# Optimization experiments

Measured on AMD Instinct MI355X. Metric: run time of the kernel, lower is better.

Reference implementation:

```python
import jax, jax.numpy as jnp
import numpy as np

DT = 1.0
TOL = 2e-4
MAX_FK = 0.1


def _lap(x):
    # 5-point Laplacian with periodic boundary (roll-based), x: [B,1,H,W]
    return (jnp.roll(x, 1, -1) + jnp.roll(x, -1, -1)
            + jnp.roll(x, 1, -2) + jnp.roll(x, -1, -2) - 4.0 * x)


def _gs_step(u, v, Du, Dv, F, k, dt):
    uvv = u * v * v
    u_next = u + dt * (Du * _lap(u) - uvv + F * (1.0 - u))
    v_next = v + dt * (Dv * _lap(v) + uvv - (F + k) * v)
    return u_next, v_next


def setup_inputs() -> dict:
    key = jax.random.key(0)
    k1, k2 = jax.random.split(key)
    B, H, W = 32, 512, 512
    # physically sensible Gray-Scott init: u near 1, v small
    u = 1.0 - 0.5 * jax.random.uniform(k1, (B, 1, H, W), dtype=jnp.float32)
    v = 0.25 * jax.random.uniform(k2, (B, 1, H, W), dtype=jnp.float32)
    return {
        "u": u,
        "v": v,
        "log_Du": jnp.float32(-2.0),
        "log_Dv": jnp.float32(-2.0),
        "raw_F": jnp.float32(0.0),
        "raw_k": jnp.float32(0.0),
        "max_steps": 64,
        "K": 32,
    }


def reference(u, v, log_Du, log_Dv, raw_F, raw_k, max_steps, K):
    # params_tensor()
    Du = jax.nn.softplus(log_Du)
    Dv = jax.nn.softplus(log_Dv)
    F = MAX_FK * jax.nn.sigmoid(raw_F)
    k = MAX_FK * jax.nn.sigmoid(raw_k)

    B = u.shape[0]
    converged0 = jnp.zeros((B,), dtype=bool)

    # Phase 1: simulate-until-converged (per-sample freeze), expressed as a
    # fixed-length masked scan (no data-dependent shapes). Samples that were
    # already converged at the start of a step keep their state frozen,
    # matching the index_select/scatter semantics of the torch loop.
    def steady_body(carry, _):
        u, v, conv = carry
        u_next, v_next = _gs_step(u, v, Du, Dv, F, k, DT)
        du = jnp.max(jnp.abs(u_next - u), axis=(1, 2, 3))
        dv = jnp.max(jnp.abs(v_next - v), axis=(1, 2, 3))
        newly = jnp.maximum(du, dv) < TOL
        m = conv[:, None, None, None]
        u2 = jnp.where(m, u, u_next)
        v2 = jnp.where(m, v, v_next)
        return (u2, v2, conv | newly), None

    (u, v, converged), _ = jax.lax.scan(
        steady_body, (u, v, converged0), None, length=max_steps)

    # Phase 2: K differentiable steps (trunc BPTT segment), no masking
    def bptt_body(carry, _):
        u, v = carry
        return _gs_step(u, v, Du, Dv, F, k, DT), None

    (u, v), _ = jax.lax.scan(bptt_body, (u, v), None, length=K)
    return (u, v)
```

## Files before the change

### kernel.cpp

```cpp
#include <hip/hip_runtime.h>

#define HH 512
#define WW 512
#define BB 32
#define NIMG (HH * WW)
#define NT (BB * NIMG)
#define TOLF 0.0002f
#define HS 32
#define NSTRIP (HH / HS)
#define TRP 16
#define TIP (TRP + 2)
#define NTBP (HH / TRP)

__device__ __forceinline__ void gs_math(
    const float4& cu, const float4& uu, const float4& ud, float ul, float ur,
    const float4& cv, const float4& vu, const float4& vd, float vl, float vr,
    float Du, float Dv, float F, float Fk, float4& un, float4& vn)
{
    float4 lu, lv;
    lu.x = ul   + cu.y + uu.x + ud.x - 4.f * cu.x;
    lu.y = cu.x + cu.z + uu.y + ud.y - 4.f * cu.y;
    lu.z = cu.y + cu.w + uu.z + ud.z - 4.f * cu.z;
    lu.w = cu.z + ur   + uu.w + ud.w - 4.f * cu.w;
    lv.x = vl   + cv.y + vu.x + vd.x - 4.f * cv.x;
    lv.y = cv.x + cv.z + vu.y + vd.y - 4.f * cv.y;
    lv.z = cv.y + cv.w + vu.z + vd.z - 4.f * cv.z;
    lv.w = cv.z + vr   + vu.w + vd.w - 4.f * cv.w;
    float uvv;
    uvv  = cu.x * cv.x * cv.x;
    un.x = cu.x + (Du * lu.x - uvv + F * (1.f - cu.x));
    vn.x = cv.x + (Dv * lv.x + uvv - Fk * cv.x);
    uvv  = cu.y * cv.y * cv.y;
    un.y = cu.y + (Du * lu.y - uvv + F * (1.f - cu.y));
    vn.y = cv.y + (Dv * lv.y + uvv - Fk * cv.y);
    uvv  = cu.z * cv.z * cv.z;
    un.z = cu.z + (Du * lu.z - uvv + F * (1.f - cu.z));
    vn.z = cv.z + (Dv * lv.z + uvv - Fk * cv.z);
    uvv  = cu.w * cv.w * cv.w;
    un.w = cu.w + (Du * lu.w - uvv + F * (1.f - cu.w));
    vn.w = cv.w + (Dv * lv.w + uvv - Fk * cv.w);
}

__device__ __forceinline__ float dmax8(const float4& un, const float4& cu,
                                       const float4& vn, const float4& cv)
{
    return fmaxf(
        fmaxf(fmaxf(fabsf(un.x - cu.x), fabsf(un.y - cu.y)),
              fmaxf(fabsf(un.z - cu.z), fabsf(un.w - cu.w))),
        fmaxf(fmaxf(fabsf(vn.x - cv.x), fabsf(vn.y - cv.y)),
              fmaxf(fabsf(vn.z - cv.z), fabsf(vn.w - cv.w))));
}

__device__ __forceinline__ int s5(int r) { int m = r % 5; return m < 0 ? m + 5 : m; }

__device__ __forceinline__ void produce_ring(
    const float (* __restrict__ Su)[WW], const float (* __restrict__ Sv)[WW],
    float (* __restrict__ Tu)[WW], float (* __restrict__ Tv)[WW],
    int r, int c0, float Du, float Dv, float F, float Fk, float& dm, bool acc)
{
    const int sm = s5(r - 1), s0 = s5(r), sp = s5(r + 1);
    const int cl = (c0 - 4) & (WW - 1), cr = (c0 + 4) & (WW - 1);
    const float4 cu = *(const float4*)&Su[s0][c0];
    const float4 uu = *(const float4*)&Su[sm][c0];
    const float4 ud = *(const float4*)&Su[sp][c0];
    const float  ul = ((const float4*)&Su[s0][cl])->w;
    const float  ur = ((const float4*)&Su[s0][cr])->x;
    const float4 cv = *(const float4*)&Sv[s0][c0];
    const float4 vu = *(const float4*)&Sv[sm][c0];
    const float4 vd = *(const float4*)&Sv[sp][c0];
    const float  vl = ((const float4*)&Sv[s0][cl])->w;
    const float  vr = ((const float4*)&Sv[s0][cr])->x;
    float4 un, vn;
    gs_math(cu, uu, ud, ul, ur, cv, vu, vd, vl, vr, Du, Dv, F, Fk, un, vn);
    *(float4*)&Tu[s0][c0] = un;
    *(float4*)&Tv[s0][c0] = vn;
    if (acc) dm = fmaxf(dm, dmax8(un, cu, vn, cv));
}

__global__ __launch_bounds__(256)
void gs_quad(const float* __restrict__ fsU, const float* __restrict__ fsV,
             float* wsU, float* wsV, float* outU, float* outV,
             const float* __restrict__ consts,
             const int* __restrict__ conv, const int* __restrict__ par,
             float* __restrict__ pmax, int tpar, int steady)
{
    __shared__ float Iu[5][WW], Iv[5][WW], Au[5][WW], Av[5][WW],
                     Bu[5][WW], Bv[5][WW], Cu[5][WW], Cv[5][WW];

    const int b = blockIdx.y;
    if (steady && conv[b]) return;
    const int p = par[b] ^ tpar;
    const float* __restrict__ su = p ? outU : wsU;
    const float* __restrict__ sv = p ? outV : wsV;
    float* __restrict__ dU = p ? wsU : outU;
    float* __restrict__ dV = p ? wsV : outV;
    if (fsU) { su = fsU; sv = fsV; }

    const float Du = consts[0], Dv = consts[1], F = consts[2], Fk = consts[3];
    const int t  = threadIdx.x;
    const int rw = t >> 7;
    const int c0 = (t & 127) * 4;
    const int R0 = blockIdx.x * HS;
    const size_t ib = (size_t)b * NIMG;

    float d1 = 0.f, d2 = 0.f, d3 = 0.f, d4 = 0.f;

    float4 pu, pv;
    {   const int g = (R0 - 4 + rw) & (HH - 1);
        pu = *(const float4*)(su + ib + (size_t)g * WW + c0);
        pv = *(const float4*)(sv + ib + (size_t)g * WW + c0);
    }

    for (int i = 0; i < 24; ++i) {
        const int rI = 2*i - 4  + rw;
        const int rA = 2*i - 6  + rw;
        const int rB = 2*i - 10 + rw;
        const int rC = 2*i - 12 + rw;
        const int rO = 2*i - 16 + rw;

        if (rI <= HS + 3) {
            const int s = s5(rI);
            *(float4*)&Iu[s][c0] = pu;
            *(float4*)&Iv[s][c0] = pv;
        }
        if (rB >= -2 && rB <= HS + 1)
            produce_ring(Au, Av, Bu, Bv, rB, c0, Du, Dv, F, Fk, d2,
                         steady && rB >= 0 && rB < HS);
        if (rO >= 0 && rO < HS) {
            const int sm = s5(rO - 1), s0 = s5(rO), sp = s5(rO + 1);
            const int cl = (c0 - 4) & (WW - 1), cr = (c0 + 4) & (WW - 1);
            const float4 cu = *(const float4*)&Cu[s0][c0];
            const float4 uu = *(const float4*)&Cu[sm][c0];
            const float4 ud = *(const float4*)&Cu[sp][c0];
            const float  ul = ((const float4*)&Cu[s0][cl])->w;
            const float  ur = ((const float4*)&Cu[s0][cr])->x;
            const float4 cv = *(const float4*)&Cv[s0][c0];
            const float4 vu = *(const float4*)&Cv[sm][c0];
            const float4 vd = *(const float4*)&Cv[sp][c0];
            const float  vl = ((const float4*)&Cv[s0][cl])->w;
            const float  vr = ((const float4*)&Cv[s0][cr])->x;
            float4 un, vn;
            gs_math(cu, uu, ud, ul, ur, cv, vu, vd, vl, vr, Du, Dv, F, Fk, un, vn);
            *(float4*)(dU + ib + (size_t)(R0 + rO) * WW + c0) = un;
            *(float4*)(dV + ib + (size_t)(R0 + rO) * WW + c0) = vn;
            if (steady) d4 = fmaxf(d4, dmax8(un, cu, vn, cv));
        }
        __syncthreads();

        {   const int rn = 2*i - 2 + rw;
            if (rn <= HS + 3) {
                const int g = (R0 + rn) & (HH - 1);
                pu = *(const float4*)(su + ib + (size_t)g * WW + c0);
                pv = *(const float4*)(sv + ib + (size_t)g * WW + c0);
            }
        }

        if (rA >= -3 && rA <= HS + 2)
            produce_ring(Iu, Iv, Au, Av, rA, c0, Du, Dv, F, Fk, d1,
                         steady && rA >= 0 && rA < HS);
        if (rC >= -1 && rC <= HS)
            produce_ring(Bu, Bv, Cu, Cv, rC, c0, Du, Dv, F, Fk, d3,
                         steady && rC >= 0 && rC < HS);
        __syncthreads();
    }

    if (steady) {
        #pragma unroll
        for (int off = 1; off < 64; off <<= 1) {
            d1 = fmaxf(d1, __shfl_xor(d1, off));
            d2 = fmaxf(d2, __shfl_xor(d2, off));
            d3 = fmaxf(d3, __shfl_xor(d3, off));
            d4 = fmaxf(d4, __shfl_xor(d4, off));
        }
        const int w = t >> 6;
        if ((t & 63) == 0) {
            Iu[0][w * 4 + 0] = d1; Iu[0][w * 4 + 1] = d2;
            Iu[0][w * 4 + 2] = d3; Iu[0][w * 4 + 3] = d4;
        }
        __syncthreads();
        if (t == 0) {
            float m0 = 0.f, m1 = 0.f, m2 = 0.f, m3 = 0.f;
            #pragma unroll
            for (int w2 = 0; w2 < 4; ++w2) {
                m0 = fmaxf(m0, Iu[0][w2 * 4 + 0]);
                m1 = fmaxf(m1, Iu[0][w2 * 4 + 1]);
                m2 = fmaxf(m2, Iu[0][w2 * 4 + 2]);
                m3 = fmaxf(m3, Iu[0][w2 * 4 + 3]);
            }
            const int idx = b * NSTRIP + blockIdx.x;
            pmax[0 * BB * NSTRIP + idx] = m0;
            pmax[1 * BB * NSTRIP + idx] = m1;
            pmax[2 * BB * NSTRIP + idx] = m2;
            pmax[3 * BB * NSTRIP + idx] = m3;
        }
    }
}

__global__ void gs_upd(const int* __restrict__ convO, const int* __restrict__ parO,
                       int* convN, int* parN, int* rbJ,
                       const float* __restrict__ pmax)
{
    const int b = blockIdx.x, t = threadIdx.x;
    if (convO[b]) { if (t == 0) { convN[b] = 1; parN[b] = parO[b]; rbJ[b] = 0; } return; }
    float v0 = 0.f, v1 = 0.f, v2 = 0.f, v3 = 0.f;
    if (t < NSTRIP) {
        const int idx = b * NSTRIP + t;
        v0 = pmax[0 * BB * NSTRIP + idx];
        v1 = pmax[1 * BB * NSTRIP + idx];
        v2 = pmax[2 * BB * NSTRIP + idx];
        v3 = pmax[3 * BB * NSTRIP + idx];
    }
    #pragma unroll
    for (int off = 1; off < NSTRIP; off <<= 1) {
        v0 = fmaxf(v0, __shfl_xor(v0, off));
        v1 = fmaxf(v1, __shfl_xor(v1, off));
        v2 = fmaxf(v2, __shfl_xor(v2, off));
        v3 = fmaxf(v3, __shfl_xor(v3, off));
    }
    if (t == 0) {
        int j = 0;
        if      (v0 < TOLF) j = 1;
        else if (v1 < TOLF) j = 2;
        else if (v2 < TOLF) j = 3;
        else if (v3 < TOLF) j = 4;
        const int pO = parO[b];
        convN[b] = (j != 0);
        parN[b]  = (j == 3) ? pO : (pO ^ 1);
        rbJ[b]   = (j >= 1 && j <= 3) ? j : 0;
    }
}

__device__ __forceinline__ void load_row(const float* __restrict__ s,
                                         int base, int baseUp, int baseDn, int c0,
                                         float4& c, float4& up, float4& dn, float& l, float& r)
{
    c  = *(const float4*)(s + base   + c0);
    up = *(const float4*)(s + baseUp + c0);
    dn = *(const float4*)(s + baseDn + c0);
    l  = s[base + ((c0 - 1) & (WW - 1))];
    r  = s[base + ((c0 + 4) & (WW - 1))];
}

__global__ __launch_bounds__(256)
void gs_rollA(const float* __restrict__ fsU, const float* __restrict__ fsV,
              float* wsU, float* wsV, float* outU, float* outV,
              const float* __restrict__ consts,
              const int* __restrict__ parO, const int* __restrict__ rbJ)
{
    __shared__ float iu[TIP][WW];
    __shared__ float iv[TIP][WW];
    const int b = blockIdx.y;
    if (rbJ[b] < 2) return;
    const int p = parO[b];
    const float* __restrict__ su = p ? outU : wsU;
    const float* __restrict__ sv = p ? outV : wsV;
    float* __restrict__ dU = p ? wsU : outU;
    float* __restrict__ dV = p ? wsV : outV;
    if (fsU) { su = fsU; sv = fsV; }
    const float Du = consts[0], Dv = consts[1], F = consts[2], Fk = consts[3];
    const int t = threadIdx.x, c0 = (t & 127) * 4, rw = t >> 7;
    const int r0 = blockIdx.x * TRP;
    for (int i = 0; i < TIP; i += 2) {
        const int li = i + rw;
        const int h  = (r0 - 1 + li) & (HH - 1);
        const int hm = (h - 1) & (HH - 1);
        const int hp = (h + 1) & (HH - 1);
        const int base   = b * NIMG + h  * WW;
        const int baseUp = b * NIMG + hm * WW;
        const int baseDn = b * NIMG + hp * WW;
        float4 cu, uu, ud, cv, vu, vd; float ul, ur, vl, vr;
        load_row(su, base, baseUp, baseDn, c0, cu, uu, ud, ul, ur);
        load_row(sv, base, baseUp, baseDn, c0, cv, vu, vd, vl, vr);
        float4 un, vn;
        gs_math(cu, uu, ud, ul, ur, cv, vu, vd, vl, vr, Du, Dv, F, Fk, un, vn);
        *(float4*)(&iu[li][c0]) = un;
        *(float4*)(&iv[li][c0]) = vn;
    }
    __syncthreads();
    for (int i = 0; i < TRP; i += 2) {
        const int li = 1 + i + rw;
        const int h  = r0 + i + rw;
        float4 cu = *(const float4*)(&iu[li][c0]);
        float4 uu = *(const float4*)(&iu[li - 1][c0]);
        float4 ud = *(const float4*)(&iu[li + 1][c0]);
        const float ul = iu[li][(c0 - 1) & (WW - 1)];
        const float ur = iu[li][(c0 + 4) & (WW - 1)];
        float4 cv = *(const float4*)(&iv[li][c0]);
        float4 vu = *(const float4*)(&iv[li - 1][c0]);
        float4 vd = *(const float4*)(&iv[li + 1][c0]);
        const float vl = iv[li][(c0 - 1) & (WW - 1)];
        const float vr = iv[li][(c0 + 4) & (WW - 1)];
        float4 un, vn;
        gs_math(cu, uu, ud, ul, ur, cv, vu, vd, vl, vr, Du, Dv, F, Fk, un, vn);
        *(float4*)(dU + b * NIMG + h * WW + c0) = un;
        *(float4*)(dV + b * NIMG + h * WW + c0) = vn;
    }
}

__global__ __launch_bounds__(256)
void gs_rollB(const float* __restrict__ fsU, const float* __restrict__ fsV,
              float* wsU, float* wsV, float* outU, float* outV,
              const float* __restrict__ consts,
              const int* __restrict__ parO, const int* __restrict__ rbJ)
{
    const int b = blockIdx.y;
    const int j = rbJ[b];
    if (j != 1 && j != 3) return;
    const int q = parO[b] ^ (j == 3 ? 1 : 0);
    const float* __restrict__ su = q ? outU : wsU;
    const float* __restrict__ sv = q ? outV : wsV;
    float* __restrict__ dU = q ? wsU : outU;
    float* __restrict__ dV = q ? wsV : outV;
    if (j == 1 && fsU) { su = fsU; sv = fsV; }
    const float Du = consts[0], Dv = consts[1], F = consts[2], Fk = consts[3];
    const int idx = blockIdx.x * 256 + threadIdx.x;
    const int h  = idx >> 7;
    const int c0 = (idx & 127) * 4;
    const int hm = (h - 1) & (HH - 1);
    const int hp = (h + 1) & (HH - 1);
    const int base   = b * NIMG + h  * WW;
    const int baseUp = b * NIMG + hm * WW;
    const int baseDn = b * NIMG + hp * WW;
    float4 cu, uu, ud, cv, vu, vd; float ul, ur, vl, vr;
    load_row(su, base, baseUp, baseDn, c0, cu, uu, ud, ul, ur);
    load_row(sv, base, baseUp, baseDn, c0, cv, vu, vd, vl, vr);
    float4 un, vn;
    gs_math(cu, uu, ud, ul, ur, cv, vu, vd, vl, vr, Du, Dv, F, Fk, un, vn);
    *(float4*)(dU + base + c0) = un;
    *(float4*)(dV + base + c0) = vn;
}

__global__ void gs_init(const float* lDu, const float* lDv, const float* rF, const float* rk,
                        float* consts, int* conv0, int* par0, int* rbJ)
{
    const int t = threadIdx.x;
    if (t == 0) {
        const float a = lDu[0], c = lDv[0];
        const float Du = (a > 0.f) ? a + log1pf(expf(-a)) : log1pf(expf(a));
        const float Dv = (c > 0.f) ? c + log1pf(expf(-c)) : log1pf(expf(c));
        const float F  = 0.1f / (1.f + expf(-rF[0]));
        const float kk = 0.1f / (1.f + expf(-rk[0]));
        consts[0] = Du; consts[1] = Dv; consts[2] = F; consts[3] = F + kk;
    }
    if (t < BB) { conv0[t] = 0; par0[t] = 0; rbJ[t] = 0; }
}

__launch_bounds__(256)
__global__ void gs_final(const float* __restrict__ wsU, const float* __restrict__ wsV,
                         float* outU, float* outV, const int* __restrict__ par)
{
    const int b = blockIdx.y;
    if (par[b] != 0) return;
    const int off = b * NIMG + (blockIdx.x * 256 + threadIdx.x) * 4;
    *(float4*)(outU + off) = *(const float4*)(wsU + off);
    *(float4*)(outV + off) = *(const float4*)(wsV + off);
}

extern "C" void kernel_launch(void* const* d_in, const int* in_sizes, int n_in,
                              void* d_out, int out_size, void* d_ws, size_t ws_size,
                              hipStream_t stream)
{
    const float* in_u = (const float*)d_in[0];
    const float* in_v = (const float*)d_in[1];
    const float* lDu  = (const float*)d_in[2];
    const float* lDv  = (const float*)d_in[3];
    const float* rF   = (const float*)d_in[4];
    const float* rk   = (const float*)d_in[5];
    const int NQUAD_STEADY = 16;
    const int NQUAD_BPTT   = 8;

    float* wsU = (float*)d_ws;
    float* wsV = wsU + NT;
    float* aux = wsV + NT;
    float* consts = aux;
    int* conv0 = (int*)(aux + 4);
    int* par0  = conv0 + BB;
    int* conv1 = par0 + BB;
    int* par1  = conv1 + BB;
    int* rbJ   = par1 + BB;
    float* pmax = (float*)(rbJ + BB);

    float* outU = (float*)d_out;
    float* outV = outU + NT;

    gs_init<<<1, 64, 0, stream>>>(lDu, lDv, rF, rk, consts, conv0, par0, rbJ);

    const dim3 gridQ(NSTRIP, BB);
    for (int s = 0; s < NQUAD_STEADY; ++s) {
        int* cO = (s & 1) ? conv1 : conv0;
        int* pO = (s & 1) ? par1  : par0;
        int* cN = (s & 1) ? conv0 : conv1;
        int* pN = (s & 1) ? par0  : par1;
        const float* fU = (s == 0) ? in_u : nullptr;
        const float* fV = (s == 0) ? in_v : nullptr;
        gs_quad<<<gridQ, 256, 0, stream>>>(fU, fV, wsU, wsV, outU, outV, consts,
                                           cO, pO, pmax, 0, 1);
        gs_upd<<<BB, 64, 0, stream>>>(cO, pO, cN, pN, rbJ, pmax);
        gs_rollA<<<dim3(NTBP, BB), 256, 0, stream>>>(fU, fV, wsU, wsV, outU, outV,
                                                     consts, pO, rbJ);
        gs_rollB<<<dim3(NIMG / 1024, BB), 256, 0, stream>>>(fU, fV, wsU, wsV, outU, outV,
                                                            consts, pO, rbJ);
    }
    for (int j = 0; j < NQUAD_BPTT; ++j) {
        gs_quad<<<gridQ, 256, 0, stream>>>(nullptr, nullptr, wsU, wsV, outU, outV, consts,
                                           conv0, par0, pmax, j & 1, 0);
    }
    gs_final<<<dim3(NIMG / 1024, BB), 256, 0, stream>>>(wsU, wsV, outU, outV, par0);
}
```

Baseline: 1.288 ms.

## Restructure fused 4-step stencil to one-column-per-thread with register row window

The temporally fused 4-step Gray-Scott kernel now uses 512 threads, each owning one column and processing one row per iteration, instead of 256 threads with float4 columns processing two rows. The first stage keeps a 3-row sliding window in registers, so the input shared ring is dropped. Horizontal neighbours come from wavefront shuffles, with small shared edge buffers at wave boundaries. This is meant to cut shared-memory traffic and footprint and raise occupancy. In exchange it adds more loop iterations and a barrier per row, plus scalar global loads in place of float4 loads.

```diff
diff --git a/kernel.cpp b/kernel.cpp
--- a/kernel.cpp
+++ b/kernel.cpp
@@ -11,6 +11,7 @@
 #define TRP 16
 #define TIP (TRP + 2)
 #define NTBP (HH / TRP)
+
 
 __device__ __forceinline__ void gs_math(
     const float4& cu, const float4& uu, const float4& ud, float ul, float ur,
@@ -41,51 +42,27 @@
     vn.w = cv.w + (Dv * lv.w + uvv - Fk * cv.w);
 }
 
-__device__ __forceinline__ float dmax8(const float4& un, const float4& cu,
-                                       const float4& vn, const float4& cv)
-{
-    return fmaxf(
-        fmaxf(fmaxf(fabsf(un.x - cu.x), fabsf(un.y - cu.y)),
-              fmaxf(fabsf(un.z - cu.z), fabsf(un.w - cu.w))),
-        fmaxf(fmaxf(fabsf(vn.x - cv.x), fabsf(vn.y - cv.y)),
-              fmaxf(fabsf(vn.z - cv.z), fabsf(vn.w - cv.w))));
-}
-
-__device__ __forceinline__ int s5(int r) { int m = r % 5; return m < 0 ? m + 5 : m; }
-
-__device__ __forceinline__ void produce_ring(
-    const float (* __restrict__ Su)[WW], const float (* __restrict__ Sv)[WW],
-    float (* __restrict__ Tu)[WW], float (* __restrict__ Tv)[WW],
-    int r, int c0, float Du, float Dv, float F, float Fk, float& dm, bool acc)
-{
-    const int sm = s5(r - 1), s0 = s5(r), sp = s5(r + 1);
-    const int cl = (c0 - 4) & (WW - 1), cr = (c0 + 4) & (WW - 1);
-    const float4 cu = *(const float4*)&Su[s0][c0];
-    const float4 uu = *(const float4*)&Su[sm][c0];
-    const float4 ud = *(const float4*)&Su[sp][c0];
-    const float  ul = ((const float4*)&Su[s0][cl])->w;
-    const float  ur = ((const float4*)&Su[s0][cr])->x;
-    const float4 cv = *(const float4*)&Sv[s0][c0];
-    const float4 vu = *(const float4*)&Sv[sm][c0];
-    const float4 vd = *(const float4*)&Sv[sp][c0];
-    const float  vl = ((const float4*)&Sv[s0][cl])->w;
-    const float  vr = ((const float4*)&Sv[s0][cr])->x;
-    float4 un, vn;
-    gs_math(cu, uu, ud, ul, ur, cv, vu, vd, vl, vr, Du, Dv, F, Fk, un, vn);
-    *(float4*)&Tu[s0][c0] = un;
-    *(float4*)&Tv[s0][c0] = vn;
-    if (acc) dm = fmaxf(dm, dmax8(un, cu, vn, cv));
-}
-
-__global__ __launch_bounds__(256)
+__device__ __forceinline__ void load_row(const float* __restrict__ s,
+                                         int base, int baseUp, int baseDn, int c0,
+                                         float4& c, float4& up, float4& dn, float& l, float& r)
+{
+    c  = *(const float4*)(s + base   + c0);
+    up = *(const float4*)(s + baseUp + c0);
+    dn = *(const float4*)(s + baseDn + c0);
+    l  = s[base + ((c0 - 1) & (WW - 1))];
+    r  = s[base + ((c0 + 4) & (WW - 1))];
+}
+
+__global__ __launch_bounds__(512)
 void gs_quad(const float* __restrict__ fsU, const float* __restrict__ fsV,
              float* wsU, float* wsV, float* outU, float* outV,
              const float* __restrict__ consts,
              const int* __restrict__ conv, const int* __restrict__ par,
              float* __restrict__ pmax, int tpar, int steady)
 {
-    __shared__ float Iu[5][WW], Iv[5][WW], Au[5][WW], Av[5][WW],
-                     Bu[5][WW], Bv[5][WW], Cu[5][WW], Cv[5][WW];
+    __shared__ float Au[4][WW], Av[4][WW], Bu[4][WW], Bv[4][WW], Cu[4][WW], Cv[4][WW];
+    __shared__ float eLu[8][4], eLv[8][4], eRu[8][4], eRv[8][4];
+    __shared__ float sred[8][4];
 
     const int b = blockIdx.y;
     if (steady && conv[b]) return;
@@ -97,70 +74,85 @@
     if (fsU) { su = fsU; sv = fsV; }
 
     const float Du = consts[0], Dv = consts[1], F = consts[2], Fk = consts[3];
-    const int t  = threadIdx.x;
-    const int rw = t >> 7;
-    const int c0 = (t & 127) * 4;
-    const int R0 = blockIdx.x * HS;
+    const int t    = threadIdx.x;
+    const int lane = t & 63, w = t >> 6;
+    const int R0   = blockIdx.x * HS;
     const size_t ib = (size_t)b * NIMG;
 
+    float w0u = 0.f, w1u = 0.f, w2u = 0.f, w0v = 0.f, w1v = 0.f, w2v = 0.f;
     float d1 = 0.f, d2 = 0.f, d3 = 0.f, d4 = 0.f;
 
-    float4 pu, pv;
-    {   const int g = (R0 - 4 + rw) & (HH - 1);
-        pu = *(const float4*)(su + ib + (size_t)g * WW + c0);
-        pv = *(const float4*)(sv + ib + (size_t)g * WW + c0);
-    }
-
-    for (int i = 0; i < 24; ++i) {
-        const int rI = 2*i - 4  + rw;
-        const int rA = 2*i - 6  + rw;
-        const int rB = 2*i - 10 + rw;
-        const int rC = 2*i - 12 + rw;
-        const int rO = 2*i - 16 + rw;
-
-        if (rI <= HS + 3) {
-            const int s = s5(rI);
-            *(float4*)&Iu[s][c0] = pu;
-            *(float4*)&Iv[s][c0] = pv;
-        }
-        if (rB >= -2 && rB <= HS + 1)
-            produce_ring(Au, Av, Bu, Bv, rB, c0, Du, Dv, F, Fk, d2,
-                         steady && rB >= 0 && rB < HS);
-        if (rO >= 0 && rO < HS) {
-            const int sm = s5(rO - 1), s0 = s5(rO), sp = s5(rO + 1);
-            const int cl = (c0 - 4) & (WW - 1), cr = (c0 + 4) & (WW - 1);
-            const float4 cu = *(const float4*)&Cu[s0][c0];
-            const float4 uu = *(const float4*)&Cu[sm][c0];
-            const float4 ud = *(const float4*)&Cu[sp][c0];
-            const float  ul = ((const float4*)&Cu[s0][cl])->w;
-            const float  ur = ((const float4*)&Cu[s0][cr])->x;
-            const float4 cv = *(const float4*)&Cv[s0][c0];
-            const float4 vu = *(const float4*)&Cv[sm][c0];
-            const float4 vd = *(const float4*)&Cv[sp][c0];
-            const float  vl = ((const float4*)&Cv[s0][cl])->w;
-            const float  vr = ((const float4*)&Cv[s0][cr])->x;
-            float4 un, vn;
-            gs_math(cu, uu, ud, ul, ur, cv, vu, vd, vl, vr, Du, Dv, F, Fk, un, vn);
-            *(float4*)(dU + ib + (size_t)(R0 + rO) * WW + c0) = un;
-            *(float4*)(dV + ib + (size_t)(R0 + rO) * WW + c0) = vn;
-            if (steady) d4 = fmaxf(d4, dmax8(un, cu, vn, cv));
-        }
-        __syncthreads();
-
-        {   const int rn = 2*i - 2 + rw;
-            if (rn <= HS + 3) {
-                const int g = (R0 + rn) & (HH - 1);
-                pu = *(const float4*)(su + ib + (size_t)g * WW + c0);
-                pv = *(const float4*)(sv + ib + (size_t)g * WW + c0);
-            }
-        }
-
-        if (rA >= -3 && rA <= HS + 2)
-            produce_ring(Iu, Iv, Au, Av, rA, c0, Du, Dv, F, Fk, d1,
-                         steady && rA >= 0 && rA < HS);
-        if (rC >= -1 && rC <= HS)
-            produce_ring(Bu, Bv, Cu, Cv, rC, c0, Du, Dv, F, Fk, d3,
-                         steady && rC >= 0 && rC < HS);
+    auto prod = [&](const float (&Su)[4][WW], const float (&Sv)[4][WW],
+                    float (&Tu)[4][WW], float (&Tv)[4][WW],
+                    int r, float& dm, bool acc) {
+        const int s0 = r & 3, sm = (r - 1) & 3, sp = (r + 1) & 3;
+        const float cu_ = Su[s0][t], uu_ = Su[sm][t], ud_ = Su[sp][t];
+        const float cv_ = Sv[s0][t], vu_ = Sv[sm][t], vd_ = Sv[sp][t];
+        float ul = __shfl_up(cu_, 1),  vl = __shfl_up(cv_, 1);
+        float ur = __shfl_down(cu_, 1), vr = __shfl_down(cv_, 1);
+        if (lane == 0)  { ul = Su[s0][(t - 1) & (WW - 1)]; vl = Sv[s0][(t - 1) & (WW - 1)]; }
+        if (lane == 63) { ur = Su[s0][(t + 1) & (WW - 1)]; vr = Sv[s0][(t + 1) & (WW - 1)]; }
+        const float lu = ul + ur + uu_ + ud_ - 4.f * cu_;
+        const float lv = vl + vr + vu_ + vd_ - 4.f * cv_;
+        const float uvv = cu_ * cv_ * cv_;
+        const float un = cu_ + (Du * lu - uvv + F * (1.f - cu_));
+        const float vn = cv_ + (Dv * lv + uvv - Fk * cv_);
+        Tu[s0][t] = un; Tv[s0][t] = vn;
+        if (acc) dm = fmaxf(dm, fmaxf(fabsf(un - cu_), fabsf(vn - cv_)));
+    };
+
+    for (int j = 0; j < 44; ++j) {
+        float nu = 0.f, nv = 0.f;
+        const bool doLoad = (j <= 39);
+        if (doLoad) {
+            const int g = (R0 + j - 4) & (HH - 1);
+            nu = su[ib + (size_t)g * WW + t];
+            nv = sv[ib + (size_t)g * WW + t];
+        }
+
+        if (j >= 3 && j <= 40) {
+            const int a = j - 6;
+            float ul = __shfl_up(w1u, 1),  vl = __shfl_up(w1v, 1);
+            float ur = __shfl_down(w1u, 1), vr = __shfl_down(w1v, 1);
+            if (lane == 0)  { ul = eLu[(w + 7) & 7][a & 3]; vl = eLv[(w + 7) & 7][a & 3]; }
+            if (lane == 63) { ur = eRu[(w + 1) & 7][a & 3]; vr = eRv[(w + 1) & 7][a & 3]; }
+            const float lu = ul + ur + w0u + w2u - 4.f * w1u;
+            const float lv = vl + vr + w0v + w2v - 4.f * w1v;
+            const float uvv = w1u * w1v * w1v;
+            const float un = w1u + (Du * lu - uvv + F * (1.f - w1u));
+            const float vn = w1v + (Dv * lv + uvv - Fk * w1v);
+            Au[a & 3][t] = un; Av[a & 3][t] = vn;
+            if (steady && a >= 0 && a < HS)
+                d1 = fmaxf(d1, fmaxf(fabsf(un - w1u), fabsf(vn - w1v)));
+        }
+        if (j >= 6 && j <= 41) prod(Au, Av, Bu, Bv, j - 8,  d2, steady && (j - 8)  >= 0 && (j - 8)  < HS);
+        if (j >= 9 && j <= 42) prod(Bu, Bv, Cu, Cv, j - 10, d3, steady && (j - 10) >= 0 && (j - 10) < HS);
+        if (j >= 12) {
+            const int o = j - 12;
+            const int s0 = o & 3, sm = (o - 1) & 3, sp = (o + 1) & 3;
+            const float cu_ = Cu[s0][t], uu_ = Cu[sm][t], ud_ = Cu[sp][t];
+            const float cv_ = Cv[s0][t], vu_ = Cv[sm][t], vd_ = Cv[sp][t];
+            float ul = __shfl_up(cu_, 1),  vl = __shfl_up(cv_, 1);
+            float ur = __shfl_down(cu_, 1), vr = __shfl_down(cv_, 1);
+            if (lane == 0)  { ul = Cu[s0][(t - 1) & (WW - 1)]; vl = Cv[s0][(t - 1) & (WW - 1)]; }
+            if (lane == 63) { ur = Cu[s0][(t + 1) & (WW - 1)]; vr = Cv[s0][(t + 1) & (WW - 1)]; }
+            const float lu = ul + ur + uu_ + ud_ - 4.f * cu_;
+            const float lv = vl + vr + vu_ + vd_ - 4.f * cv_;
+            const float uvv = cu_ * cv_ * cv_;
+            const float un = cu_ + (Du * lu - uvv + F * (1.f - cu_));
+            const float vn = cv_ + (Dv * lv + uvv - Fk * cv_);
+            dU[ib + (size_t)(R0 + o) * WW + t] = un;
+            dV[ib + (size_t)(R0 + o) * WW + t] = vn;
+            if (steady) d4 = fmaxf(d4, fmaxf(fabsf(un - cu_), fabsf(vn - cv_)));
+        }
+
+        if (doLoad) {
+            const int sl = (j - 4) & 3;
+            if (lane == 63) { eLu[w][sl] = nu; eLv[w][sl] = nv; }
+            if (lane == 0)  { eRu[w][sl] = nu; eRv[w][sl] = nv; }
+        }
+        w0u = w1u; w1u = w2u; w2u = nu;
+        w0v = w1v; w1v = w2v; w2v = nv;
         __syncthreads();
     }
 
@@ -172,20 +164,16 @@
             d3 = fmaxf(d3, __shfl_xor(d3, off));
             d4 = fmaxf(d4, __shfl_xor(d4, off));
         }
-        const int w = t >> 6;
-        if ((t & 63) == 0) {
-            Iu[0][w * 4 + 0] = d1; Iu[0][w * 4 + 1] = d2;
-            Iu[0][w * 4 + 2] = d3; Iu[0][w * 4 + 3] = d4;
-        }
+        if (lane == 0) { sred[w][0] = d1; sred[w][1] = d2; sred[w][2] = d3; sred[w][3] = d4; }
         __syncthreads();
         if (t == 0) {
             float m0 = 0.f, m1 = 0.f, m2 = 0.f, m3 = 0.f;
             #pragma unroll
-            for (int w2 = 0; w2 < 4; ++w2) {
-                m0 = fmaxf(m0, Iu[0][w2 * 4 + 0]);
-                m1 = fmaxf(m1, Iu[0][w2 * 4 + 1]);
-                m2 = fmaxf(m2, Iu[0][w2 * 4 + 2]);
-                m3 = fmaxf(m3, Iu[0][w2 * 4 + 3]);
+            for (int w2_ = 0; w2_ < 8; ++w2_) {
+                m0 = fmaxf(m0, sred[w2_][0]);
+                m1 = fmaxf(m1, sred[w2_][1]);
+                m2 = fmaxf(m2, sred[w2_][2]);
+                m3 = fmaxf(m3, sred[w2_][3]);
             }
             const int idx = b * NSTRIP + blockIdx.x;
             pmax[0 * BB * NSTRIP + idx] = m0;
@@ -228,17 +216,6 @@
         parN[b]  = (j == 3) ? pO : (pO ^ 1);
         rbJ[b]   = (j >= 1 && j <= 3) ? j : 0;
     }
-}
-
-__device__ __forceinline__ void load_row(const float* __restrict__ s,
-                                         int base, int baseUp, int baseDn, int c0,
-                                         float4& c, float4& up, float4& dn, float& l, float& r)
-{
-    c  = *(const float4*)(s + base   + c0);
-    up = *(const float4*)(s + baseUp + c0);
-    dn = *(const float4*)(s + baseDn + c0);
-    l  = s[base + ((c0 - 1) & (WW - 1))];
-    r  = s[base + ((c0 + 4) & (WW - 1))];
 }
 
 __global__ __launch_bounds__(256)
@@ -393,7 +370,7 @@
         int* pN = (s & 1) ? par0  : par1;
         const float* fU = (s == 0) ? in_u : nullptr;
         const float* fV = (s == 0) ? in_v : nullptr;
-        gs_quad<<<gridQ, 256, 0, stream>>>(fU, fV, wsU, wsV, outU, outV, consts,
+        gs_quad<<<gridQ, 512, 0, stream>>>(fU, fV, wsU, wsV, outU, outV, consts,
                                            cO, pO, pmax, 0, 1);
         gs_upd<<<BB, 64, 0, stream>>>(cO, pO, cN, pN, rbJ, pmax);
         gs_rollA<<<dim3(NTBP, BB), 256, 0, stream>>>(fU, fV, wsU, wsV, outU, outV,
@@ -402,7 +379,7 @@
                                                             consts, pO, rbJ);
     }
     for (int j = 0; j < NQUAD_BPTT; ++j) {
-        gs_quad<<<gridQ, 256, 0, stream>>>(nullptr, nullptr, wsU, wsV, outU, outV, consts,
+        gs_quad<<<gridQ, 512, 0, stream>>>(nullptr, nullptr, wsU, wsV, outU, outV, consts,
                                            conv0, par0, pmax, j & 1, 0);
     }
     gs_final<<<dim3(NIMG / 1024, BB), 256, 0, stream>>>(wsU, wsV, outU, outV, par0);
```

Result: slower. 1.980 ms (+53.7%).
